# Kernel optimization log

Hardware: AMD Instinct MI355X
Metric: run time of the kernel (lower is better)

The kernel has to match this reference:

```python
import jax, jax.numpy as jnp
import numpy as np

N = 50000      # nodes
E = 640000     # edges
D = 128        # input_dim
H = 128        # hidden_channels
L = 2          # n_layers
NG = 512       # number of graphs
NC = 1         # n_classes
BN_EPS = 1e-5


def _bn(x, gamma, beta):
    # BatchNorm1d over node dim, batch statistics (biased var), eps=1e-5
    mu = jnp.mean(x, axis=0)
    var = jnp.mean((x - mu) ** 2, axis=0)
    return (x - mu) * jax.lax.rsqrt(var + BN_EPS) * gamma + beta


def setup_inputs() -> dict:
    key = jax.random.key(0)
    ks = jax.random.split(key, 16)
    s = 0.05
    x = jax.random.normal(ks[0], (N, D), dtype=jnp.float32)
    edge_index = jax.random.randint(ks[1], (2, E), 0, N, dtype=jnp.int64)
    batch = jnp.sort(jax.random.randint(ks[2], (N,), 0, NG, dtype=jnp.int64))
    return {
        "x": x,
        "edge_index": edge_index,
        "batch": batch,
        "lin_in_w": jax.random.normal(ks[3], (D, H), dtype=jnp.float32) * s,
        "lin_in_b": jnp.zeros((H,), dtype=jnp.float32),
        "mlp_w1": jax.random.normal(ks[4], (L, H, H), dtype=jnp.float32) * s,
        "mlp_b1": jnp.zeros((L, H), dtype=jnp.float32),
        "bn1_g": jnp.ones((L, H), dtype=jnp.float32),
        "bn1_b": jnp.zeros((L, H), dtype=jnp.float32),
        "mlp_w2": jax.random.normal(ks[5], (L, H, H), dtype=jnp.float32) * s,
        "mlp_b2": jnp.zeros((L, H), dtype=jnp.float32),
        "bn_g": jnp.ones((L, H), dtype=jnp.float32),
        "bn_b": jnp.zeros((L, H), dtype=jnp.float32),
        "jk_w": jax.random.normal(ks[6], (L * H, NC), dtype=jnp.float32) * s,
        "jk_b": jnp.zeros((NC,), dtype=jnp.float32),
    }


def reference(x, edge_index, batch, lin_in_w, lin_in_b, mlp_w1, mlp_b1,
              bn1_g, bn1_b, mlp_w2, mlp_b2, bn_g, bn_b, jk_w, jk_b):
    src, dst = edge_index[0], edge_index[1]
    n = x.shape[0]
    h = x @ lin_in_w + lin_in_b  # [N, H]
    outs = []
    for l in range(mlp_w1.shape[0]):
        # GINConv (eps=0): mlp(x + sum_{j in N(i)} x_j)
        agg = jax.ops.segment_sum(h[src], dst, num_segments=n)
        z = h + agg
        z = z @ mlp_w1[l] + mlp_b1[l]
        z = jax.nn.relu(_bn(z, bn1_g[l], bn1_b[l]))
        z = z @ mlp_w2[l] + mlp_b2[l]
        # outer BatchNorm + ReLU; dropout is identity in eval
        h = jax.nn.relu(_bn(z, bn_g[l], bn_b[l]))
        outs.append(h)
    hcat = jnp.concatenate(outs, axis=-1)  # [N, L*H]
    # global mean pool per graph
    counts = jax.ops.segment_sum(jnp.ones((n,), dtype=hcat.dtype), batch, num_segments=NG)
    pooled = jax.ops.segment_sum(hcat, batch, num_segments=NG)
    pooled = pooled / jnp.maximum(counts, 1.0)[:, None]
    return pooled @ jk_w + jk_b  # [NG, n_classes]
```

## Files before the change

### kernel.cpp

```cpp
#include <hip/hip_runtime.h>
#include <cstddef>

#define NN 50000
#define NE 640000
#define NG 512
#define NL 2
#define NSLOT 16
constexpr float BN_EPS = 1e-5f;

typedef __attribute__((ext_vector_type(8))) short bf16x8;
typedef __attribute__((ext_vector_type(16))) float f32x16;

__device__ inline float b2f_lo(unsigned int u) {
  union { unsigned int i; float f; } v; v.i = u << 16; return v.f;
}
__device__ inline float b2f_hi(unsigned int u) {
  union { unsigned int i; float f; } v; v.i = u & 0xffff0000u; return v.f;
}
__device__ inline unsigned short f2b(float f) {
  union { float f; unsigned int i; } v; v.f = f;
  return (unsigned short)((v.i + 0x7fffu + ((v.i >> 16) & 1u)) >> 16);
}
__device__ inline unsigned int pack2(float lo, float hi) {
  return (unsigned int)f2b(lo) | ((unsigned int)f2b(hi) << 16);
}
__device__ inline int swz(int row, int b) { return row * 256 + (b ^ ((row & 15) << 4)); }

__device__ inline void unpack_add(const uint4 v, float* a) {
  a[0] += b2f_lo(v.x); a[1] += b2f_hi(v.x); a[2] += b2f_lo(v.y); a[3] += b2f_hi(v.y);
  a[4] += b2f_lo(v.z); a[5] += b2f_hi(v.z); a[6] += b2f_lo(v.w); a[7] += b2f_hi(v.w);
}

__global__ __launch_bounds__(256) void gemm_gather32(
    const unsigned short* __restrict__ h, const int* __restrict__ rowptr,
    const int* __restrict__ srcs, const unsigned short* __restrict__ Wt,
    const float* __restrict__ bias, unsigned short* __restrict__ C,
    float* __restrict__ psum, float* __restrict__ psq, int n) {
  __shared__ uint4 Au[16][32];
  __shared__ float colsum[128];
  __shared__ float colsq[128];
  const int t = threadIdx.x;
  const int row0 = blockIdx.x * 32;

  if (t < 128) { colsum[t] = 0.f; colsq[t] = 0.f; }

  const int ln = t & 31;
  const int cg = t >> 5;
  const int gr = row0 + ln;
  const uint4* h4 = (const uint4*)h;
  float a0[8], a1[8];
  #pragma unroll
  for (int p = 0; p < 8; ++p) { a0[p] = 0.f; a1[p] = 0.f; }
  if (gr < n) {
    {
      const uint4* p = &h4[(size_t)gr * 16 + cg * 2];
      unpack_add(p[0], a0); unpack_add(p[1], a1);
    }
    const int beg = rowptr[gr], end = rowptr[gr + 1];
    int j = beg;
    for (; j + 1 < end; j += 2) {
      const uint4* p0 = &h4[(size_t)srcs[j] * 16 + cg * 2];
      const uint4* p1 = &h4[(size_t)srcs[j + 1] * 16 + cg * 2];
      const uint4 v00 = p0[0], v01 = p0[1];
      const uint4 v10 = p1[0], v11 = p1[1];
      unpack_add(v00, a0); unpack_add(v01, a1);
      unpack_add(v10, a0); unpack_add(v11, a1);
    }
    if (j < end) {
      const uint4* p0 = &h4[(size_t)srcs[j] * 16 + cg * 2];
      unpack_add(p0[0], a0); unpack_add(p0[1], a1);
    }
  }
  {
    uint4 o0, o1;
    o0.x = pack2(a0[0], a0[1]); o0.y = pack2(a0[2], a0[3]);
    o0.z = pack2(a0[4], a0[5]); o0.w = pack2(a0[6], a0[7]);
    o1.x = pack2(a1[0], a1[1]); o1.y = pack2(a1[2], a1[3]);
    o1.z = pack2(a1[4], a1[5]); o1.w = pack2(a1[6], a1[7]);
    Au[cg * 2][ln] = o0;
    Au[cg * 2 + 1][ln] = o1;
  }
  __syncthreads();

  const int w = t >> 6;
  const int l = t & 63;
  const int lane31 = l & 31;
  const int khalf = l >> 5;

  f32x16 acc;
  #pragma unroll
  for (int i = 0; i < 16; ++i) acc[i] = 0.f;

  const unsigned short* Bp = Wt + (size_t)(w * 32 + lane31) * 128 + 8 * khalf;
  #pragma unroll
  for (int k0 = 0; k0 < 8; ++k0) {
    const bf16x8 aF = *(const bf16x8*)&Au[k0 * 2 + khalf][lane31];
    const bf16x8 bF = *(const bf16x8*)(Bp + k0 * 16);
    acc = __builtin_amdgcn_mfma_f32_32x32x16_bf16(aF, bF, acc, 0, 0, 0);
  }

  const int col = w * 32 + lane31;
  const float bs = bias[col];
  float s0 = 0.f, q0 = 0.f;
  #pragma unroll
  for (int r = 0; r < 16; ++r) {
    const int row = (r & 3) + 8 * (r >> 2) + 4 * khalf;
    const int grow = row0 + row;
    if (grow < n) {
      const float v = acc[r] + bs;
      C[(size_t)grow * 128 + col] = f2b(v);
      s0 += v; q0 = fmaf(v, v, q0);
    }
  }
  atomicAdd(&colsum[col], s0);
  atomicAdd(&colsq[col], q0);
  __syncthreads();
  if (t < 128) {
    const int slot = blockIdx.x & (NSLOT - 1);
    atomicAdd(&psum[slot * 128 + t], colsum[t]);
    atomicAdd(&psq[slot * 128 + t], colsq[t]);
  }
}

template <int MODE, bool STATS>
__global__ __launch_bounds__(256) void gemm_fused(
    const void* __restrict__ Ain, const float* __restrict__ scale,
    const float* __restrict__ shift, const unsigned short* __restrict__ Wt,
    const float* __restrict__ bias, unsigned short* __restrict__ C,
    float* __restrict__ psum, float* __restrict__ psq, int n) {
  __shared__ char Al[16384];
  __shared__ float colsum[128];
  __shared__ float colsq[128];
  const int t = threadIdx.x;
  const int row0 = blockIdx.x * 64;

  if (STATS && t < 128) { colsum[t] = 0.f; colsq[t] = 0.f; }

  #pragma unroll
  for (int ii = 0; ii < 4; ++ii) {
    const int i = t + ii * 256;
    const int r = i >> 4;
    const int u = (i & 15) << 4;
    const int gr = row0 + r;
    uint4 v = make_uint4(0u, 0u, 0u, 0u);
    if (gr < n) {
      if (MODE == 3) {
        const float* Af = (const float*)Ain;
        const float4 f0 = *(const float4*)(Af + (size_t)gr * 128 + (u >> 1));
        const float4 f1 = *(const float4*)(Af + (size_t)gr * 128 + (u >> 1) + 4);
        v.x = pack2(f0.x, f0.y); v.y = pack2(f0.z, f0.w);
        v.z = pack2(f1.x, f1.y); v.w = pack2(f1.z, f1.w);
      } else {
        v = *(const uint4*)((const char*)Ain + (size_t)gr * 256 + u);
        const int c0 = u >> 1;
        unsigned int pw[4] = {v.x, v.y, v.z, v.w};
        #pragma unroll
        for (int p = 0; p < 4; ++p) {
          float lo = b2f_lo(pw[p]);
          float hi = b2f_hi(pw[p]);
          lo = fmaxf(fmaf(lo, scale[c0 + 2 * p], shift[c0 + 2 * p]), 0.f);
          hi = fmaxf(fmaf(hi, scale[c0 + 2 * p + 1], shift[c0 + 2 * p + 1]), 0.f);
          pw[p] = pack2(lo, hi);
        }
        v = make_uint4(pw[0], pw[1], pw[2], pw[3]);
      }
    }
    *(uint4*)(Al + swz(r, u)) = v;
  }
  __syncthreads();

  const int w = t >> 6;
  const int l = t & 63;
  const int lane31 = l & 31;
  const int khalf = l >> 5;
  const int mrow = (w & 1) * 32;
  const int c0 = (w >> 1) * 64;

  f32x16 acc0, acc1;
  #pragma unroll
  for (int i = 0; i < 16; ++i) { acc0[i] = 0.f; acc1[i] = 0.f; }

  const unsigned short* Bp0 = Wt + (size_t)(c0 + lane31) * 128 + 8 * khalf;
  const unsigned short* Bp1 = Wt + (size_t)(c0 + 32 + lane31) * 128 + 8 * khalf;

  #pragma unroll
  for (int k0 = 0; k0 < 128; k0 += 16) {
    const int kb = (k0 + 8 * khalf) * 2;
    const bf16x8 a  = *(const bf16x8*)(Al + swz(mrow + lane31, kb));
    const bf16x8 b0 = *(const bf16x8*)(Bp0 + k0);
    const bf16x8 b1 = *(const bf16x8*)(Bp1 + k0);
    acc0 = __builtin_amdgcn_mfma_f32_32x32x16_bf16(a, b0, acc0, 0, 0, 0);
    acc1 = __builtin_amdgcn_mfma_f32_32x32x16_bf16(a, b1, acc1, 0, 0, 0);
  }

  const float bias0 = bias[c0 + lane31];
  const float bias1 = bias[c0 + 32 + lane31];
  float s0 = 0.f, q0 = 0.f, s1 = 0.f, q1 = 0.f;
  #pragma unroll
  for (int r = 0; r < 16; ++r) {
    const int row = mrow + (r & 3) + 8 * (r >> 2) + 4 * khalf;
    const int grow = row0 + row;
    if (grow < n) {
      const float v0 = acc0[r] + bias0;
      const float v1 = acc1[r] + bias1;
      C[(size_t)grow * 128 + c0 + lane31] = f2b(v0);
      C[(size_t)grow * 128 + c0 + 32 + lane31] = f2b(v1);
      if (STATS) {
        s0 += v0; q0 = fmaf(v0, v0, q0);
        s1 += v1; q1 = fmaf(v1, v1, q1);
      }
    }
  }
  if (STATS) {
    atomicAdd(&colsum[c0 + lane31], s0);
    atomicAdd(&colsq[c0 + lane31], q0);
    atomicAdd(&colsum[c0 + 32 + lane31], s1);
    atomicAdd(&colsq[c0 + 32 + lane31], q1);
    __syncthreads();
    if (t < 128) {
      const int slot = blockIdx.x & (NSLOT - 1);
      atomicAdd(&psum[slot * 128 + t], colsum[t]);
      atomicAdd(&psq[slot * 128 + t], colsq[t]);
    }
  }
}

__global__ __launch_bounds__(256) void conv_w_k(
    const float* __restrict__ lw, const float* __restrict__ w1,
    const float* __restrict__ w2, unsigned short* __restrict__ Wt) {
  const int i = blockIdx.x * 256 + threadIdx.x;
  if (i >= 5 * 16384) return;
  const int m = i >> 14, r = i & 16383;
  const int ncol = r >> 7, k = r & 127;
  const float* src = (m == 0) ? lw : (m <= 2) ? (w1 + (m - 1) * 16384)
                                              : (w2 + (m - 3) * 16384);
  Wt[i] = f2b(src[k * 128 + ncol]);
}

#define SCAN_B 196
__global__ __launch_bounds__(256) void edge_hist(const int* __restrict__ ei,
                                                 int* __restrict__ cnt) {
  const int e = blockIdx.x * 256 + threadIdx.x;
  if (e >= NE) return;
  atomicAdd(&cnt[ei[NE + e]], 1);
}

__global__ __launch_bounds__(256) void scan1(const int* __restrict__ cnt,
                                             int* __restrict__ rowptr,
                                             int* __restrict__ bsum) {
  __shared__ int s[256];
  const int b = blockIdx.x, t = threadIdx.x;
  const int i = b * 256 + t;
  const int v = (i < NN) ? cnt[i] : 0;
  s[t] = v;
  __syncthreads();
  for (int off = 1; off < 256; off <<= 1) {
    const int x = (t >= off) ? s[t - off] : 0;
    __syncthreads();
    s[t] += x;
    __syncthreads();
  }
  if (i < NN) rowptr[i] = s[t] - v;
  if (t == 255) bsum[b] = s[255];
}

__global__ __launch_bounds__(256) void scan2(const int* __restrict__ bsum,
                                             int* __restrict__ boff,
                                             int* __restrict__ rowptrN) {
  __shared__ int s[256];
  const int t = threadIdx.x;
  const int v = (t < SCAN_B) ? bsum[t] : 0;
  s[t] = v;
  __syncthreads();
  for (int off = 1; off < 256; off <<= 1) {
    const int x = (t >= off) ? s[t - off] : 0;
    __syncthreads();
    s[t] += x;
    __syncthreads();
  }
  if (t < SCAN_B) boff[t] = s[t] - v;
  if (t == 255) *rowptrN = s[255];
}

__global__ __launch_bounds__(256) void scan3(int* __restrict__ rowptr,
                                             const int* __restrict__ boff,
                                             int* __restrict__ cursor) {
  const int i = blockIdx.x * 256 + threadIdx.x;
  if (i < NN) {
    const int v = rowptr[i] + boff[blockIdx.x];
    rowptr[i] = v;
    cursor[i] = v;
  }
}

__global__ __launch_bounds__(256) void build_csr(const int* __restrict__ ei,
                                                 int* __restrict__ cursor,
                                                 int* __restrict__ srcs) {
  const int e = blockIdx.x * 256 + threadIdx.x;
  if (e >= NE) return;
  const int src = ei[e];
  const int dst = ei[NE + e];
  const int pos = atomicAdd(&cursor[dst], 1);
  srcs[pos] = src;
}

__global__ void bn_stats_final(const float* __restrict__ psum,
                               const float* __restrict__ psq,
                               const float* __restrict__ gamma,
                               const float* __restrict__ beta,
                               float* __restrict__ scale,
                               float* __restrict__ shift, int n) {
  const int c = threadIdx.x;
  float s = 0.f, s2 = 0.f;
  #pragma unroll
  for (int b = 0; b < NSLOT; ++b) {
    s += psum[b * 128 + c];
    s2 += psq[b * 128 + c];
  }
  const float inv_n = 1.f / (float)n;
  const float mu = s * inv_n;
  float var = s2 * inv_n - mu * mu;
  var = fmaxf(var, 0.f);
  const float sc = rsqrtf(var + BN_EPS) * gamma[c];
  scale[c] = sc;
  shift[c] = beta[c] - mu * sc;
}

template <bool WRITE_H>
__global__ __launch_bounds__(256) void bn_relu_pool_seg_b(
    const unsigned short* __restrict__ Z, const float* __restrict__ scale,
    const float* __restrict__ shift, const int* __restrict__ gstart,
    unsigned short* __restrict__ h, float* __restrict__ pooled, int layerOff) {
  const int g = blockIdx.x;
  const int r0 = gstart[g], r1 = gstart[g + 1];
  const int t = threadIdx.x;
  const int q = t & 15;
  const int rr = t >> 4;
  const int c0 = q * 8;
  float sc[8], sh[8], acc[8];
  #pragma unroll
  for (int i = 0; i < 8; ++i) { sc[i] = scale[c0 + i]; sh[i] = shift[c0 + i]; acc[i] = 0.f; }
  for (int r = r0 + rr; r < r1; r += 16) {
    const uint4 v = ((const uint4*)Z)[(size_t)r * 16 + q];
    float o[8];
    o[0] = b2f_lo(v.x); o[1] = b2f_hi(v.x); o[2] = b2f_lo(v.y); o[3] = b2f_hi(v.y);
    o[4] = b2f_lo(v.z); o[5] = b2f_hi(v.z); o[6] = b2f_lo(v.w); o[7] = b2f_hi(v.w);
    #pragma unroll
    for (int i = 0; i < 8; ++i) {
      o[i] = fmaxf(fmaf(o[i], sc[i], sh[i]), 0.f);
      acc[i] += o[i];
    }
    if (WRITE_H) {
      uint4 ov;
      ov.x = pack2(o[0], o[1]); ov.y = pack2(o[2], o[3]);
      ov.z = pack2(o[4], o[5]); ov.w = pack2(o[6], o[7]);
      ((uint4*)h)[(size_t)r * 16 + q] = ov;
    }
  }
  __shared__ float red[256 * 8];
  #pragma unroll
  for (int i = 0; i < 8; ++i) red[t * 8 + i] = acc[i];
  __syncthreads();
  for (int off = 8; off >= 1; off >>= 1) {
    if (rr < off) {
      #pragma unroll
      for (int i = 0; i < 8; ++i)
        red[t * 8 + i] += red[(t + off * 16) * 8 + i];
    }
    __syncthreads();
  }
  if (rr == 0) {
    #pragma unroll
    for (int i = 0; i < 8; ++i)
      pooled[(size_t)g * 256 + layerOff + c0 + i] = red[t * 8 + i];
  }
}

__global__ void compute_segments(const int* __restrict__ batch,
                                 int* __restrict__ gstart,
                                 float* __restrict__ counts) {
  const int g = blockIdx.x * blockDim.x + threadIdx.x;
  if (g > NG) return;
  int lo = 0, hi = NN;
  while (lo < hi) { int m = (lo + hi) >> 1; if (batch[m] < g) lo = m + 1; else hi = m; }
  gstart[g] = lo;
  if (g < NG) {
    int lo1 = lo, hi1 = NN;
    while (lo1 < hi1) { int m = (lo1 + hi1) >> 1; if (batch[m] < g + 1) lo1 = m + 1; else hi1 = m; }
    counts[g] = (float)(lo1 - lo);
  }
}

__global__ __launch_bounds__(256) void final_out(
    const float* __restrict__ pooled, const float* __restrict__ counts,
    const float* __restrict__ jkw, const float* __restrict__ jkb,
    float* __restrict__ out) {
  const int wave = threadIdx.x >> 6;
  const int lane = threadIdx.x & 63;
  const int g = blockIdx.x * 4 + wave;
  if (g >= NG) return;
  const float4 p = ((const float4*)(pooled + (size_t)g * 256))[lane];
  const float4 w = ((const float4*)jkw)[lane];
  float s = p.x * w.x + p.y * w.y + p.z * w.z + p.w * w.w;
  for (int off = 32; off; off >>= 1) s += __shfl_down(s, off, 64);
  if (lane == 0) out[g] = s / fmaxf(counts[g], 1.f) + jkb[0];
}

extern "C" void kernel_launch(void* const* d_in, const int* in_sizes, int n_in,
                              void* d_out, int out_size, void* d_ws,
                              size_t ws_size, hipStream_t stream) {
  const float* x     = (const float*)d_in[0];
  const int*   ei    = (const int*)d_in[1];
  const int*   batch = (const int*)d_in[2];
  const float* lin_w = (const float*)d_in[3];
  const float* lin_b = (const float*)d_in[4];
  const float* w1    = (const float*)d_in[5];
  const float* b1    = (const float*)d_in[6];
  const float* g1    = (const float*)d_in[7];
  const float* be1   = (const float*)d_in[8];
  const float* w2    = (const float*)d_in[9];
  const float* b2    = (const float*)d_in[10];
  const float* g2    = (const float*)d_in[11];
  const float* be2   = (const float*)d_in[12];
  const float* jkw   = (const float*)d_in[13];
  const float* jkb   = (const float*)d_in[14];
  float* out = (float*)d_out;

  char* base = (char*)d_ws;
  unsigned short* hb  = (unsigned short*)base;
  unsigned short* agb = hb + (size_t)NN * 128;
  unsigned short* WtA = agb + (size_t)NN * 128;
  float* scale  = (float*)(WtA + 5 * 16384);
  float* shift  = scale + 128;
  float* pooled = shift + 128;
  float* counts = pooled + (size_t)NG * 256;
  int* gstart = (int*)(counts + NG);
  int* rowptr = gstart + NG + 4;
  int* bsum   = rowptr + NN + 4;
  int* boff   = bsum + 200;
  int* srcs   = boff + 200;
  int* cnt    = srcs + NE;
  float* stats = (float*)(cnt + NN);

  hipMemsetAsync(cnt, 0, (size_t)NN * sizeof(int) + 4 * 4096 * sizeof(float),
                 stream);
  conv_w_k<<<(5 * 16384 + 255) / 256, 256, 0, stream>>>(lin_w, w1, w2, WtA);
  compute_segments<<<3, 256, 0, stream>>>(batch, gstart, counts);

  edge_hist<<<(NE + 255) / 256, 256, 0, stream>>>(ei, cnt);
  scan1<<<SCAN_B, 256, 0, stream>>>(cnt, rowptr, bsum);
  scan2<<<1, 256, 0, stream>>>(bsum, boff, rowptr + NN);
  scan3<<<SCAN_B, 256, 0, stream>>>(rowptr, boff, cnt);
  build_csr<<<(NE + 255) / 256, 256, 0, stream>>>(ei, cnt, srcs);

  const int gemm_grid = (NN + 63) / 64;
  const int gath_grid = (NN + 31) / 32;

  gemm_fused<3, false><<<gemm_grid, 256, 0, stream>>>(
      x, nullptr, nullptr, WtA, lin_b, hb, nullptr, nullptr, NN);

  for (int l = 0; l < NL; ++l) {
    float* st1 = stats + (l * 2 + 0) * 4096;
    float* st2 = stats + (l * 2 + 1) * 4096;
    gemm_gather32<<<gath_grid, 256, 0, stream>>>(
        hb, rowptr, srcs, WtA + (1 + l) * 16384, b1 + l * 128, agb,
        st1, st1 + 2048, NN);
    bn_stats_final<<<1, 128, 0, stream>>>(st1, st1 + 2048, g1 + l * 128,
                                          be1 + l * 128, scale, shift, NN);
    gemm_fused<2, true><<<gemm_grid, 256, 0, stream>>>(
        agb, scale, shift, WtA + (3 + l) * 16384, b2 + l * 128, agb,
        st2, st2 + 2048, NN);
    bn_stats_final<<<1, 128, 0, stream>>>(st2, st2 + 2048, g2 + l * 128,
                                          be2 + l * 128, scale, shift, NN);
    if (l + 1 < NL) {
      bn_relu_pool_seg_b<true><<<NG, 256, 0, stream>>>(
          agb, scale, shift, gstart, hb, pooled, l * 128);
    } else {
      bn_relu_pool_seg_b<false><<<NG, 256, 0, stream>>>(
          agb, scale, shift, gstart, hb, pooled, l * 128);
    }
  }

  final_out<<<NG / 4, 256, 0, stream>>>(pooled, counts, jkw, jkb, out);
}
```

Measured before the change: 258.7 us.

## Fold BN finalize into consumers and apply layer-1 BN/ReLU inside gather

```diff
diff --git a/kernel.cpp b/kernel.cpp
--- a/kernel.cpp
+++ b/kernel.cpp
@@ -30,31 +30,80 @@
   a[0] += b2f_lo(v.x); a[1] += b2f_hi(v.x); a[2] += b2f_lo(v.y); a[3] += b2f_hi(v.y);
   a[4] += b2f_lo(v.z); a[5] += b2f_hi(v.z); a[6] += b2f_lo(v.w); a[7] += b2f_hi(v.w);
 }
-
+__device__ inline void unpack_bn_add(const uint4 v, float* a, const float* sc,
+                                     const float* sh) {
+  a[0] += fmaxf(fmaf(b2f_lo(v.x), sc[0], sh[0]), 0.f);
+  a[1] += fmaxf(fmaf(b2f_hi(v.x), sc[1], sh[1]), 0.f);
+  a[2] += fmaxf(fmaf(b2f_lo(v.y), sc[2], sh[2]), 0.f);
+  a[3] += fmaxf(fmaf(b2f_hi(v.y), sc[3], sh[3]), 0.f);
+  a[4] += fmaxf(fmaf(b2f_lo(v.z), sc[4], sh[4]), 0.f);
+  a[5] += fmaxf(fmaf(b2f_hi(v.z), sc[5], sh[5]), 0.f);
+  a[6] += fmaxf(fmaf(b2f_lo(v.w), sc[6], sh[6]), 0.f);
+  a[7] += fmaxf(fmaf(b2f_hi(v.w), sc[7], sh[7]), 0.f);
+}
+
+__device__ inline void bn_from_stats(const float* __restrict__ st,
+                                     const float* __restrict__ gamma,
+                                     const float* __restrict__ beta, int c,
+                                     float& sc, float& sh) {
+  float s = 0.f, s2 = 0.f;
+  #pragma unroll
+  for (int b = 0; b < NSLOT; ++b) {
+    s += st[b * 128 + c];
+    s2 += st[2048 + b * 128 + c];
+  }
+  const float inv_n = 1.f / (float)NN;
+  const float mu = s * inv_n;
+  const float var = fmaxf(s2 * inv_n - mu * mu, 0.f);
+  sc = rsqrtf(var + BN_EPS) * gamma[c];
+  sh = beta[c] - mu * sc;
+}
+
+template <bool BN>
 __global__ __launch_bounds__(256) void gemm_gather32(
     const unsigned short* __restrict__ h, const int* __restrict__ rowptr,
-    const int* __restrict__ srcs, const unsigned short* __restrict__ Wt,
-    const float* __restrict__ bias, unsigned short* __restrict__ C,
-    float* __restrict__ psum, float* __restrict__ psq, int n) {
+    const int* __restrict__ srcs, const float* __restrict__ stIn,
+    const float* __restrict__ gIn, const float* __restrict__ beIn,
+    const unsigned short* __restrict__ Wt, const float* __restrict__ bias,
+    unsigned short* __restrict__ C, float* __restrict__ psum,
+    float* __restrict__ psq, int n) {
   __shared__ uint4 Au[16][32];
   __shared__ float colsum[128];
   __shared__ float colsq[128];
+  __shared__ float sc_s[128], sh_s[128];
   const int t = threadIdx.x;
   const int row0 = blockIdx.x * 32;
 
-  if (t < 128) { colsum[t] = 0.f; colsq[t] = 0.f; }
+  if (t < 128) {
+    colsum[t] = 0.f; colsq[t] = 0.f;
+    if (BN) {
+      float a, b;
+      bn_from_stats(stIn, gIn, beIn, t, a, b);
+      sc_s[t] = a; sh_s[t] = b;
+    }
+  }
+  if (BN) __syncthreads();
 
   const int ln = t & 31;
   const int cg = t >> 5;
   const int gr = row0 + ln;
   const uint4* h4 = (const uint4*)h;
   float a0[8], a1[8];
+  float sc0[8], sh0[8], sc1[8], sh1[8];
   #pragma unroll
   for (int p = 0; p < 8; ++p) { a0[p] = 0.f; a1[p] = 0.f; }
+  if (BN) {
+    #pragma unroll
+    for (int p = 0; p < 8; ++p) {
+      sc0[p] = sc_s[cg * 16 + p];     sh0[p] = sh_s[cg * 16 + p];
+      sc1[p] = sc_s[cg * 16 + 8 + p]; sh1[p] = sh_s[cg * 16 + 8 + p];
+    }
+  }
   if (gr < n) {
     {
       const uint4* p = &h4[(size_t)gr * 16 + cg * 2];
-      unpack_add(p[0], a0); unpack_add(p[1], a1);
+      if (BN) { unpack_bn_add(p[0], a0, sc0, sh0); unpack_bn_add(p[1], a1, sc1, sh1); }
+      else    { unpack_add(p[0], a0); unpack_add(p[1], a1); }
     }
     const int beg = rowptr[gr], end = rowptr[gr + 1];
     int j = beg;
@@ -63,12 +112,18 @@
       const uint4* p1 = &h4[(size_t)srcs[j + 1] * 16 + cg * 2];
       const uint4 v00 = p0[0], v01 = p0[1];
       const uint4 v10 = p1[0], v11 = p1[1];
-      unpack_add(v00, a0); unpack_add(v01, a1);
-      unpack_add(v10, a0); unpack_add(v11, a1);
+      if (BN) {
+        unpack_bn_add(v00, a0, sc0, sh0); unpack_bn_add(v01, a1, sc1, sh1);
+        unpack_bn_add(v10, a0, sc0, sh0); unpack_bn_add(v11, a1, sc1, sh1);
+      } else {
+        unpack_add(v00, a0); unpack_add(v01, a1);
+        unpack_add(v10, a0); unpack_add(v11, a1);
+      }
     }
     if (j < end) {
       const uint4* p0 = &h4[(size_t)srcs[j] * 16 + cg * 2];
-      unpack_add(p0[0], a0); unpack_add(p0[1], a1);
+      if (BN) { unpack_bn_add(p0[0], a0, sc0, sh0); unpack_bn_add(p0[1], a1, sc1, sh1); }
+      else    { unpack_add(p0[0], a0); unpack_add(p0[1], a1); }
     }
   }
   {
@@ -124,17 +179,27 @@
 
 template <int MODE, bool STATS>
 __global__ __launch_bounds__(256) void gemm_fused(
-    const void* __restrict__ Ain, const float* __restrict__ scale,
-    const float* __restrict__ shift, const unsigned short* __restrict__ Wt,
-    const float* __restrict__ bias, unsigned short* __restrict__ C,
-    float* __restrict__ psum, float* __restrict__ psq, int n) {
+    const void* __restrict__ Ain, const float* __restrict__ stIn,
+    const float* __restrict__ gIn, const float* __restrict__ beIn,
+    const unsigned short* __restrict__ Wt, const float* __restrict__ bias,
+    unsigned short* __restrict__ C, float* __restrict__ psum,
+    float* __restrict__ psq, int n) {
   __shared__ char Al[16384];
   __shared__ float colsum[128];
   __shared__ float colsq[128];
+  __shared__ float sc_s[128], sh_s[128];
   const int t = threadIdx.x;
   const int row0 = blockIdx.x * 64;
 
-  if (STATS && t < 128) { colsum[t] = 0.f; colsq[t] = 0.f; }
+  if (t < 128) {
+    if (STATS) { colsum[t] = 0.f; colsq[t] = 0.f; }
+    if (MODE == 2) {
+      float a, b;
+      bn_from_stats(stIn, gIn, beIn, t, a, b);
+      sc_s[t] = a; sh_s[t] = b;
+    }
+  }
+  if (MODE == 2) __syncthreads();
 
   #pragma unroll
   for (int ii = 0; ii < 4; ++ii) {
@@ -158,8 +223,8 @@
         for (int p = 0; p < 4; ++p) {
           float lo = b2f_lo(pw[p]);
           float hi = b2f_hi(pw[p]);
-          lo = fmaxf(fmaf(lo, scale[c0 + 2 * p], shift[c0 + 2 * p]), 0.f);
-          hi = fmaxf(fmaf(hi, scale[c0 + 2 * p + 1], shift[c0 + 2 * p + 1]), 0.f);
+          lo = fmaxf(fmaf(lo, sc_s[c0 + 2 * p], sh_s[c0 + 2 * p]), 0.f);
+          hi = fmaxf(fmaf(hi, sc_s[c0 + 2 * p + 1], sh_s[c0 + 2 * p + 1]), 0.f);
           pw[p] = pack2(lo, hi);
         }
         v = make_uint4(pw[0], pw[1], pw[2], pw[3]);
@@ -225,16 +290,37 @@
   }
 }
 
-__global__ __launch_bounds__(256) void conv_w_k(
+__global__ __launch_bounds__(256) void setup_k(
     const float* __restrict__ lw, const float* __restrict__ w1,
-    const float* __restrict__ w2, unsigned short* __restrict__ Wt) {
-  const int i = blockIdx.x * 256 + threadIdx.x;
-  if (i >= 5 * 16384) return;
-  const int m = i >> 14, r = i & 16383;
-  const int ncol = r >> 7, k = r & 127;
-  const float* src = (m == 0) ? lw : (m <= 2) ? (w1 + (m - 1) * 16384)
-                                              : (w2 + (m - 3) * 16384);
-  Wt[i] = f2b(src[k * 128 + ncol]);
+    const float* __restrict__ w2, unsigned short* __restrict__ Wt,
+    const int* __restrict__ batch, int* __restrict__ gstart,
+    float* __restrict__ counts, int* __restrict__ cnt,
+    float* __restrict__ stats) {
+  const int b = blockIdx.x, t = threadIdx.x;
+  if (b < 320) {
+    const int i = b * 256 + t;
+    const int m = i >> 14, r = i & 16383;
+    const int ncol = r >> 7, k = r & 127;
+    const float* src = (m == 0) ? lw : (m <= 2) ? (w1 + (m - 1) * 16384)
+                                                : (w2 + (m - 3) * 16384);
+    Wt[i] = f2b(src[k * 128 + ncol]);
+  } else if (b < 516) {
+    const int i = (b - 320) * 256 + t;
+    if (i < NN) cnt[i] = 0;
+  } else if (b < 580) {
+    stats[(b - 516) * 256 + t] = 0.f;
+  } else {
+    const int g = (b - 580) * 256 + t;
+    if (g > NG) return;
+    int lo = 0, hi = NN;
+    while (lo < hi) { int m = (lo + hi) >> 1; if (batch[m] < g) lo = m + 1; else hi = m; }
+    gstart[g] = lo;
+    if (g < NG) {
+      int lo1 = lo, hi1 = NN;
+      while (lo1 < hi1) { int m = (lo1 + hi1) >> 1; if (batch[m] < g + 1) lo1 = m + 1; else hi1 = m; }
+      counts[g] = (float)(lo1 - lo);
+    }
+  }
 }
 
 #define SCAN_B 196
@@ -304,58 +390,34 @@
   srcs[pos] = src;
 }
 
-__global__ void bn_stats_final(const float* __restrict__ psum,
-                               const float* __restrict__ psq,
-                               const float* __restrict__ gamma,
-                               const float* __restrict__ beta,
-                               float* __restrict__ scale,
-                               float* __restrict__ shift, int n) {
-  const int c = threadIdx.x;
-  float s = 0.f, s2 = 0.f;
-  #pragma unroll
-  for (int b = 0; b < NSLOT; ++b) {
-    s += psum[b * 128 + c];
-    s2 += psq[b * 128 + c];
-  }
-  const float inv_n = 1.f / (float)n;
-  const float mu = s * inv_n;
-  float var = s2 * inv_n - mu * mu;
-  var = fmaxf(var, 0.f);
-  const float sc = rsqrtf(var + BN_EPS) * gamma[c];
-  scale[c] = sc;
-  shift[c] = beta[c] - mu * sc;
-}
-
-template <bool WRITE_H>
 __global__ __launch_bounds__(256) void bn_relu_pool_seg_b(
-    const unsigned short* __restrict__ Z, const float* __restrict__ scale,
-    const float* __restrict__ shift, const int* __restrict__ gstart,
-    unsigned short* __restrict__ h, float* __restrict__ pooled, int layerOff) {
+    const unsigned short* __restrict__ Z, const float* __restrict__ stIn,
+    const float* __restrict__ gIn, const float* __restrict__ beIn,
+    const int* __restrict__ gstart, float* __restrict__ pooled, int layerOff) {
+  __shared__ float sc_s[128], sh_s[128];
   const int g = blockIdx.x;
+  const int t = threadIdx.x;
+  if (t < 128) {
+    float a, b;
+    bn_from_stats(stIn, gIn, beIn, t, a, b);
+    sc_s[t] = a; sh_s[t] = b;
+  }
+  __syncthreads();
   const int r0 = gstart[g], r1 = gstart[g + 1];
-  const int t = threadIdx.x;
   const int q = t & 15;
   const int rr = t >> 4;
   const int c0 = q * 8;
   float sc[8], sh[8], acc[8];
   #pragma unroll
-  for (int i = 0; i < 8; ++i) { sc[i] = scale[c0 + i]; sh[i] = shift[c0 + i]; acc[i] = 0.f; }
+  for (int i = 0; i < 8; ++i) { sc[i] = sc_s[c0 + i]; sh[i] = sh_s[c0 + i]; acc[i] = 0.f; }
   for (int r = r0 + rr; r < r1; r += 16) {
     const uint4 v = ((const uint4*)Z)[(size_t)r * 16 + q];
     float o[8];
     o[0] = b2f_lo(v.x); o[1] = b2f_hi(v.x); o[2] = b2f_lo(v.y); o[3] = b2f_hi(v.y);
     o[4] = b2f_lo(v.z); o[5] = b2f_hi(v.z); o[6] = b2f_lo(v.w); o[7] = b2f_hi(v.w);
     #pragma unroll
-    for (int i = 0; i < 8; ++i) {
-      o[i] = fmaxf(fmaf(o[i], sc[i], sh[i]), 0.f);
-      acc[i] += o[i];
-    }
-    if (WRITE_H) {
-      uint4 ov;
-      ov.x = pack2(o[0], o[1]); ov.y = pack2(o[2], o[3]);
-      ov.z = pack2(o[4], o[5]); ov.w = pack2(o[6], o[7]);
-      ((uint4*)h)[(size_t)r * 16 + q] = ov;
-    }
+    for (int i = 0; i < 8; ++i)
+      acc[i] += fmaxf(fmaf(o[i], sc[i], sh[i]), 0.f);
   }
   __shared__ float red[256 * 8];
   #pragma unroll
@@ -373,21 +435,6 @@
     #pragma unroll
     for (int i = 0; i < 8; ++i)
       pooled[(size_t)g * 256 + layerOff + c0 + i] = red[t * 8 + i];
-  }
-}
-
-__global__ void compute_segments(const int* __restrict__ batch,
-                                 int* __restrict__ gstart,
-                                 float* __restrict__ counts) {
-  const int g = blockIdx.x * blockDim.x + threadIdx.x;
-  if (g > NG) return;
-  int lo = 0, hi = NN;
-  while (lo < hi) { int m = (lo + hi) >> 1; if (batch[m] < g) lo = m + 1; else hi = m; }
-  gstart[g] = lo;
-  if (g < NG) {
-    int lo1 = lo, hi1 = NN;
-    while (lo1 < hi1) { int m = (lo1 + hi1) >> 1; if (batch[m] < g + 1) lo1 = m + 1; else hi1 = m; }
-    counts[g] = (float)(lo1 - lo);
   }
 }
 
@@ -430,9 +477,7 @@
   unsigned short* hb  = (unsigned short*)base;
   unsigned short* agb = hb + (size_t)NN * 128;
   unsigned short* WtA = agb + (size_t)NN * 128;
-  float* scale  = (float*)(WtA + 5 * 16384);
-  float* shift  = scale + 128;
-  float* pooled = shift + 128;
+  float* pooled = (float*)(WtA + 5 * 16384);
   float* counts = pooled + (size_t)NG * 256;
   int* gstart = (int*)(counts + NG);
   int* rowptr = gstart + NG + 4;
@@ -442,10 +487,8 @@
   int* cnt    = srcs + NE;
   float* stats = (float*)(cnt + NN);
 
-  hipMemsetAsync(cnt, 0, (size_t)NN * sizeof(int) + 4 * 4096 * sizeof(float),
-                 stream);
-  conv_w_k<<<(5 * 16384 + 255) / 256, 256, 0, stream>>>(lin_w, w1, w2, WtA);
-  compute_segments<<<3, 256, 0, stream>>>(batch, gstart, counts);
+  setup_k<<<583, 256, 0, stream>>>(lin_w, w1, w2, WtA, batch, gstart, counts,
+                                   cnt, stats);
 
   edge_hist<<<(NE + 255) / 256, 256, 0, stream>>>(ei, cnt);
   scan1<<<SCAN_B, 256, 0, stream>>>(cnt, rowptr, bsum);
@@ -456,30 +499,31 @@
   const int gemm_grid = (NN + 63) / 64;
   const int gath_grid = (NN + 31) / 32;
 
+  float* st1_0 = stats;
+  float* st2_0 = stats + 4096;
+  float* st1_1 = stats + 2 * 4096;
+  float* st2_1 = stats + 3 * 4096;
+
   gemm_fused<3, false><<<gemm_grid, 256, 0, stream>>>(
-      x, nullptr, nullptr, WtA, lin_b, hb, nullptr, nullptr, NN);
-
-  for (int l = 0; l < NL; ++l) {
-    float* st1 = stats + (l * 2 + 0) * 4096;
-    float* st2 = stats + (l * 2 + 1) * 4096;
-    gemm_gather32<<<gath_grid, 256, 0, stream>>>(
-        hb, rowptr, srcs, WtA + (1 + l) * 16384, b1 + l * 128, agb,
-        st1, st1 + 2048, NN);
-    bn_stats_final<<<1, 128, 0, stream>>>(st1, st1 + 2048, g1 + l * 128,
-                                          be1 + l * 128, scale, shift, NN);
-    gemm_fused<2, true><<<gemm_grid, 256, 0, stream>>>(
-        agb, scale, shift, WtA + (3 + l) * 16384, b2 + l * 128, agb,
-        st2, st2 + 2048, NN);
-    bn_stats_final<<<1, 128, 0, stream>>>(st2, st2 + 2048, g2 + l * 128,
-                                          be2 + l * 128, scale, shift, NN);
-    if (l + 1 < NL) {
-      bn_relu_pool_seg_b<true><<<NG, 256, 0, stream>>>(
-          agb, scale, shift, gstart, hb, pooled, l * 128);
-    } else {
-      bn_relu_pool_seg_b<false><<<NG, 256, 0, stream>>>(
-          agb, scale, shift, gstart, hb, pooled, l * 128);
-    }
-  }
+      x, nullptr, nullptr, nullptr, WtA, lin_b, hb, nullptr, nullptr, NN);
+
+  gemm_gather32<false><<<gath_grid, 256, 0, stream>>>(
+      hb, rowptr, srcs, nullptr, nullptr, nullptr, WtA + 1 * 16384,
+      b1, agb, st1_0, st1_0 + 2048, NN);
+  gemm_fused<2, true><<<gemm_grid, 256, 0, stream>>>(
+      agb, st1_0, g1, be1, WtA + 3 * 16384, b2, agb,
+      st2_0, st2_0 + 2048, NN);
+  bn_relu_pool_seg_b<<<NG, 256, 0, stream>>>(agb, st2_0, g2, be2, gstart,
+                                             pooled, 0);
+
+  gemm_gather32<true><<<gath_grid, 256, 0, stream>>>(
+      agb, rowptr, srcs, st2_0, g2, be2, WtA + 2 * 16384,
+      b1 + 128, hb, st1_1, st1_1 + 2048, NN);
+  gemm_fused<2, true><<<gemm_grid, 256, 0, stream>>>(
+      hb, st1_1, g1 + 128, be1 + 128, WtA + 4 * 16384, b2 + 128, hb,
+      st2_1, st2_1 + 2048, NN);
+  bn_relu_pool_seg_b<<<NG, 256, 0, stream>>>(hb, st2_1, g2 + 128, be2 + 128,
+                                             gstart, pooled, 128);
 
   final_out<<<NG / 4, 256, 0, stream>>>(pooled, counts, jkw, jkb, out);
 }
```

Result: faster. 252.7 us (-2.3%).
